# Performance work log

Hardware: AMD Instinct MI355X
Metric: run time of the kernel (lower is better)

Reference implementation:

```python
import jax, jax.numpy as jnp
import numpy as np

# Static configuration (matches init_kwargs)
L = 3264          # seq_length
K = 12            # ktc=4 -> K=12
LOCC = 4          # ktc=4 -> Locc=4
S, B, A = 8, 64, 4  # streams (user/port pairs), batch, rx antennas
DELAY_MIN, DELAY_MAX = -10, 10


def _phasor(m):
    # m: integer shifts [S, B] -> exp(1j*2*pi*m*n/L) as [S, B, L]
    n = jnp.arange(L, dtype=jnp.int32)
    ang = (2.0 * np.pi / L) * ((m[..., None] * n) % L).astype(jnp.float32)
    return jax.lax.complex(jnp.cos(ang), jnp.sin(ang))


def _linear_interp(h_avg):
    # np.interp with uniform source grid orig[i] = (LOCC-1)/2 + i*LOCC, clamped at ends.
    # h_avg: [S, B, A, R] complex, R = L // LOCC -> [S, B, A, L]
    R = L // LOCC
    new = jnp.arange(L, dtype=jnp.float32)
    t = jnp.clip((new - (LOCC - 1) / 2.0) / LOCC, 0.0, float(R - 1))
    i0 = jnp.floor(t).astype(jnp.int32)
    i1 = jnp.minimum(i0 + 1, R - 1)
    frac = (t - i0).astype(jnp.float32)
    return h_avg[..., i0] * (1.0 - frac) + h_avg[..., i1] * frac


def reference(ls_real, ls_imag, cyclic_shifts, noise_powers):
    ls = jax.lax.complex(ls_real, ls_imag)                     # [S,B,A,L]
    ideal_peak = ((K - cyclic_shifts) % K) * (L // K)          # [S]

    # Stage 1: IFFT + timing-offset search (torch.no_grad in original)
    h_time = jnp.fft.ifft(ls, axis=-1)
    power = jax.lax.stop_gradient(jnp.sum(jnp.abs(h_time) ** 2, axis=2))  # [S,B,L]
    offs = jnp.arange(DELAY_MIN, DELAY_MAX + 1, dtype=jnp.int32)          # [21]
    cand_idx = (ideal_peak[:, None] + offs[None, :]) % L                   # [S,21]
    cand_idx = jnp.broadcast_to(cand_idx[:, None, :], (S, B, offs.shape[0]))
    cand_pow = jnp.take_along_axis(power, cand_idx, axis=-1)               # [S,B,21]
    t_off = offs[jnp.argmax(cand_pow, axis=-1)]                            # [S,B]
    m = t_off + ideal_peak[:, None]                                        # [S,B]
    ph_m = _phasor(m)        # [S,B,L]
    ph_T = _phasor(t_off)    # [S,B,L]

    # Stage 2: phasor shift, OCC demux, interpolation (inside no_grad in original)
    h_shift = ls * ph_m[:, :, None, :]
    h_avg = h_shift.reshape(S, B, A, L // LOCC, LOCC).mean(-1)             # [S,B,A,L/4]
    h_interp = jax.lax.stop_gradient(_linear_interp(h_avg))                # [S,B,A,L]

    # Stage 3: global residual against stream (0,0)'s LS estimate
    total_recon = jnp.sum(h_interp * jnp.conj(ph_m)[:, :, None, :], axis=0)  # [B,A,L]
    residual = ls[0] - total_recon                                           # [B,A,L]

    # Stage 4: apply residual, MMSE (identity: mmse_module=None), timing recovery
    h_wr = h_interp + residual[None, :, :, None, :].squeeze(3) if False else h_interp + residual[None] * ph_m[:, :, None, :]
    final = h_wr * jnp.conj(ph_T)[:, :, None, :]                             # [S,B,A,L]
    return jnp.stack([final.real, final.imag]).astype(jnp.float32)          # [2,S,B,A,L]


def setup_inputs() -> dict:
    key = jax.random.key(0)
    k1, k2, k3, k4 = jax.random.split(key, 4)
    return {
        "ls_real": jax.random.normal(k1, (S, B, A, L), dtype=jnp.float32),
        "ls_imag": jax.random.normal(k2, (S, B, A, L), dtype=jnp.float32),
        "cyclic_shifts": jax.random.randint(k3, (S,), 0, K, dtype=jnp.int32),
        "noise_powers": jax.random.uniform(k4, (B,), dtype=jnp.float32),
    }
```

## Files before the change

### kernel.cpp

```cpp
#include <hip/hip_runtime.h>

namespace {

constexpr int L = 3264;
constexpr int K = 12;
constexpr int S = 8;
constexpr int B = 64;
constexpr int A = 4;
constexpr int R = 816;
constexpr int NOFF = 21;
constexpr int PEAK_STEP = L / K;
constexpr float TWO_PI = 6.28318530717958647692f;
constexpr float CINV = TWO_PI / (float)L;
constexpr int NCHUNK = (L + 255) / 256;
constexpr int HS_MAX = 66;

__device__ __forceinline__ float rfl(float x) {
    return __uint_as_float(__builtin_amdgcn_readfirstlane(__float_as_uint(x)));
}

__device__ __forceinline__ float2 cmul(float2 a, float2 b) {
    return make_float2(a.x * b.x - a.y * b.y, a.x * b.y + a.y * b.x);
}

__global__ __launch_bounds__(256)
void k_tables(const int* __restrict__ cs,
              float2* __restrict__ phT, float2* __restrict__ phI)
{
    const int g = blockIdx.x * 256 + threadIdx.x;
    if (g < NOFF * L) {
        const int t = g / L, l = g - t * L;
        int j = ((t - 10) * l) % L; if (j < 0) j += L;
        float sv, cv; __sincosf(CINV * (float)j, &sv, &cv);
        phT[g] = make_float2(cv, sv);
    } else if (g < (NOFF + S) * L) {
        const int q = g - NOFF * L;
        const int s = q / L, l = q - s * L;
        const int ideal = ((K - cs[s]) % K) * PEAK_STEP;
        const int j = (ideal * l) % L;
        float sv, cv; __sincosf(CINV * (float)j, &sv, &cv);
        phI[q] = make_float2(cv, sv);
    }
}

template <int NB>
__device__ __forceinline__ void dft_bins(
    const float* __restrict__ lscr, const float* __restrict__ lsci,
    int idx0d0, int grouplane, int lane, int w, float2 (*red)[11])
{
    const int jb = (grouplane * idx0d0) % L;
    float br, bi; __sincosf(CINV * (float)jb, &bi, &br);
    float lr, li; __sincosf(CINV * (float)grouplane, &li, &lr);
    float pwr[NB], pwi[NB], ar[NB], ai[NB];
    pwr[0] = br; pwi[0] = bi;
    #pragma unroll
    for (int d = 1; d < NB; ++d) {
        pwr[d] = pwr[d-1] * lr - pwi[d-1] * li;
        pwi[d] = pwr[d-1] * li + pwi[d-1] * lr;
    }
    #pragma unroll
    for (int d = 0; d < NB; ++d) { ar[d] = 0.f; ai[d] = 0.f; }

    const int js = (256 * idx0d0) % L;
    float s0r, s0i; __sincosf(CINV * (float)js, &s0i, &s0r);
    float c8r, c8i; __sincosf(CINV * 256.0f, &c8i, &c8r);
    float str_[NB], sti_[NB];
    {
        float cr = s0r, ci = s0i;
        #pragma unroll
        for (int d = 0; d < NB; ++d) {
            str_[d] = rfl(cr); sti_[d] = rfl(ci);
            const float nr2 = cr * c8r - ci * c8i;
            ci = cr * c8i + ci * c8r;
            cr = nr2;
        }
    }

    for (int it = 0; it < 12; ++it) {
        const int k = grouplane + (it << 8);
        const float xr = lscr[k];
        const float xi = lsci[k];
        #pragma unroll
        for (int d = 0; d < NB; ++d) {
            ar[d] += xr * pwr[d] - xi * pwi[d];
            ai[d] += xr * pwi[d] + xi * pwr[d];
            const float nr2 = pwr[d] * str_[d] - pwi[d] * sti_[d];
            pwi[d] = pwr[d] * sti_[d] + pwi[d] * str_[d];
            pwr[d] = nr2;
        }
    }
    if (grouplane < 192) {
        const float xr = lscr[grouplane + 3072];
        const float xi = lsci[grouplane + 3072];
        #pragma unroll
        for (int d = 0; d < NB; ++d) {
            ar[d] += xr * pwr[d] - xi * pwi[d];
            ai[d] += xr * pwi[d] + xi * pwr[d];
        }
    }

    #pragma unroll
    for (int d = 0; d < NB; ++d) {
        float r = ar[d], im = ai[d];
        #pragma unroll
        for (int o = 32; o > 0; o >>= 1) {
            r  += __shfl_xor(r, o);
            im += __shfl_xor(im, o);
        }
        if (lane == 0) red[w][d] = make_float2(r, im);
    }
}

__global__ __launch_bounds__(512)
void k_dft(const float* __restrict__ lsr, const float* __restrict__ lsi,
           const int* __restrict__ cs, float* __restrict__ pow_out)
{
    __shared__ float lscr[L];
    __shared__ float lsci[L];
    __shared__ float2 red[8][11];

    const int row = blockIdx.x;
    const int sb = row >> 2;
    const int a = row & 3;
    const int s = sb >> 6;
    const int tid = threadIdx.x;
    const int lane = tid & 63;
    const int w = tid >> 6;
    const int grouplane = tid & 255;
    const int grp = tid >> 8;

    {
        const float4* __restrict__ pr4 = (const float4*)(lsr + (size_t)row * L);
        const float4* __restrict__ pi4 = (const float4*)(lsi + (size_t)row * L);
        for (int idx = tid; idx < L / 4; idx += 512) {
            const float4 r4 = pr4[idx];
            const float4 i4 = pi4[idx];
            ((float4*)lscr)[idx] = r4;
            ((float4*)lsci)[idx] = i4;
        }
    }
    __syncthreads();

    const int ideal = ((K - cs[s]) % K) * PEAK_STEP;
    int idx0 = (ideal - 10) % L; if (idx0 < 0) idx0 += L;
    const int d0 = grp ? 10 : 0;
    const int idx0d0 = (idx0 + d0) % L;

    if (grp) dft_bins<11>(lscr, lsci, idx0d0, grouplane, lane, w, red);
    else     dft_bins<10>(lscr, lsci, idx0d0, grouplane, lane, w, red);
    __syncthreads();

    if (tid < NOFF) {
        const int d = tid;
        const int g = (d < 10) ? 0 : 1;
        const int dl = d - g * 10;
        float rr = 0.f, ii = 0.f;
        #pragma unroll
        for (int q = 0; q < 4; ++q) {
            rr += red[4 * g + q][dl].x;
            ii += red[4 * g + q][dl].y;
        }
        pow_out[sb * (NOFF * A) + d * A + a] = rr * rr + ii * ii;
    }
}

__global__ __launch_bounds__(64)
void k_argmax(const float* __restrict__ pow_in, const int* __restrict__ cs,
              int* __restrict__ toff_out)
{
    const int sb = blockIdx.x;
    const int lane = threadIdx.x;

    float pw = -1.f;
    if (lane < NOFF) {
        const float4 p4 = *(const float4*)(pow_in + sb * (NOFF * A) + lane * A);
        pw = p4.x + p4.y + p4.z + p4.w;
    }
    float mx = pw;
    #pragma unroll
    for (int o = 32; o > 0; o >>= 1) mx = fmaxf(mx, __shfl_xor(mx, o));
    const unsigned long long msk = __ballot(pw == mx);
    const int argd = __ffsll(msk) - 1;
    if (lane == 0) toff_out[sb] = argd - 10;
}

__global__ __launch_bounds__(256)
void k_final(const float* __restrict__ lsr, const float* __restrict__ lsi,
             const int* __restrict__ toff_arr,
             const float2* __restrict__ phT, const float2* __restrict__ phI,
             float* __restrict__ out)
{
    __shared__ float2 hs[S][HS_MAX];
    __shared__ float2 emp_s[S];
    __shared__ int tfs[S];

    const int bid = blockIdx.x;
    const int chunk = bid % NCHUNK;
    const int ba = bid / NCHUNK;
    const int b = ba >> 2;
    const int a = ba & 3;
    const int tid = threadIdx.x;

    if (tid < S) {
        const int tf = toff_arr[tid * B + b] + 10;
        tfs[tid] = tf;
        emp_s[tid] = cmul(phI[tid * L + 1], phT[tf * L + 1]);
    }
    __syncthreads();

    const int imin = max(0, chunk * 64 - 1);
    const int imax = min(R - 1, chunk * 64 + 64);
    const int cnt = imax - imin + 1;

    for (int t = tid; t < S * HS_MAX; t += 256) {
        const int s = t / HS_MAX;
        const int ii = t - s * HS_MAX;
        if (ii < cnt) {
            const int i = imin + ii;
            const int sb = s * B + b;
            const float2 emp = emp_s[s];
            float2 w2 = cmul(phI[s * L + 4 * i], phT[tfs[s] * L + 4 * i]);
            const float4 xr = *(const float4*)(lsr + ((size_t)sb * A + a) * L + 4 * i);
            const float4 xi = *(const float4*)(lsi + ((size_t)sb * A + a) * L + 4 * i);
            float wr = w2.x, wi = w2.y;
            float are, aim, nr;
            are  = xr.x * wr - xi.x * wi;  aim  = xr.x * wi + xi.x * wr;
            nr = wr * emp.x - wi * emp.y;  wi = wr * emp.y + wi * emp.x;  wr = nr;
            are += xr.y * wr - xi.y * wi;  aim += xr.y * wi + xi.y * wr;
            nr = wr * emp.x - wi * emp.y;  wi = wr * emp.y + wi * emp.x;  wr = nr;
            are += xr.z * wr - xi.z * wi;  aim += xr.z * wi + xi.z * wr;
            nr = wr * emp.x - wi * emp.y;  wi = wr * emp.y + wi * emp.x;  wr = nr;
            are += xr.w * wr - xi.w * wi;  aim += xr.w * wi + xi.w * wr;
            hs[s][ii] = make_float2(are * 0.25f, aim * 0.25f);
        }
    }
    __syncthreads();

    const int l = chunk * 256 + tid;
    if (l >= L) return;

    float t2 = ((float)l - 1.5f) * 0.25f;
    t2 = fminf(fmaxf(t2, 0.0f), (float)(R - 1));
    const int i0 = (int)t2;
    const int i1 = min(i0 + 1, R - 1);
    const float frac = t2 - (float)i0;

    float hire[S], hiim[S], pmre[S], pmim[S], ptre[S], ptim[S];
    float rre = 0.f, rim = 0.f;

    #pragma unroll
    for (int s = 0; s < S; ++s) {
        const float2 pt = phT[tfs[s] * L + l];
        const float2 wm = cmul(phI[s * L + l], pt);
        const float2 h0 = hs[s][i0 - imin];
        const float2 h1 = hs[s][i1 - imin];
        const float hr = h0.x * (1.f - frac) + h1.x * frac;
        const float hi = h0.y * (1.f - frac) + h1.y * frac;
        hire[s] = hr; hiim[s] = hi;
        pmre[s] = wm.x; pmim[s] = wm.y;
        ptre[s] = pt.x; ptim[s] = pt.y;
        rre += hr * wm.x + hi * wm.y;
        rim += hi * wm.x - hr * wm.y;
    }

    const size_t off0 = ((size_t)(b * A + a)) * L + l;
    const float resre = lsr[off0] - rre;
    const float resim = lsi[off0] - rim;

    #pragma unroll
    for (int s = 0; s < S; ++s) {
        const float wre = hire[s] + resre * pmre[s] - resim * pmim[s];
        const float wim = hiim[s] + resre * pmim[s] + resim * pmre[s];
        const float fre = wre * ptre[s] + wim * ptim[s];
        const float fim = wim * ptre[s] - wre * ptim[s];
        const size_t o = (((size_t)(s * B + b)) * A + a) * L + l;
        __builtin_nontemporal_store(fre, &out[o]);
        __builtin_nontemporal_store(fim, &out[(size_t)S * B * A * L + o]);
    }
}

}

extern "C" void kernel_launch(void* const* d_in, const int* in_sizes, int n_in,
                              void* d_out, int out_size, void* d_ws, size_t ws_size,
                              hipStream_t stream) {
    (void)in_sizes; (void)n_in; (void)out_size; (void)ws_size;
    const float* lsr = (const float*)d_in[0];
    const float* lsi = (const float*)d_in[1];
    const int*   cs  = (const int*)d_in[2];

    int* toff = (int*)d_ws;
    float2* phT  = (float2*)((char*)d_ws + 4096);
    float2* phI  = (float2*)((char*)d_ws + 4096 + 548352);
    float*  powb = (float*)((char*)d_ws + 786432);

    const int ntab = ((NOFF + S) * L + 255) / 256;
    k_tables<<<ntab, 256, 0, stream>>>(cs, phT, phI);
    k_dft   <<<S * B * A, 512, 0, stream>>>(lsr, lsi, cs, powb);
    k_argmax<<<S * B, 64, 0, stream>>>(powb, cs, toff);
    k_final <<<B * A * NCHUNK, 256, 0, stream>>>(lsr, lsi, toff, phT, phI,
                                                 (float*)d_out);
}
```

Before: 186.0 us.

## Drop shared-memory staging in DFT and final kernels, use twiddle tables

The DFT kernel no longer stages each LS row in LDS. It reads the inputs straight from global memory and builds its twiddle factors from precomputed phasor and twiddle tables (a new L-entry table is added), with per-bin steps broadcast through readlane. The final kernel drops the shared h_avg tile and its barriers, so each thread recomputes its two interpolation neighbours per stream directly from global memory. Nontemporal stores are replaced by plain stores. This removes LDS traffic and synchronisation but adds redundant global loads and arithmetic, since neighbouring threads recompute the same h_avg entries and group 0 now does 11 bins instead of 10.

```diff
diff --git a/kernel.cpp b/kernel.cpp
--- a/kernel.cpp
+++ b/kernel.cpp
@@ -13,19 +13,18 @@
 constexpr float TWO_PI = 6.28318530717958647692f;
 constexpr float CINV = TWO_PI / (float)L;
 constexpr int NCHUNK = (L + 255) / 256;
-constexpr int HS_MAX = 66;
-
-__device__ __forceinline__ float rfl(float x) {
-    return __uint_as_float(__builtin_amdgcn_readfirstlane(__float_as_uint(x)));
-}
 
 __device__ __forceinline__ float2 cmul(float2 a, float2 b) {
     return make_float2(a.x * b.x - a.y * b.y, a.x * b.y + a.y * b.x);
 }
 
+__device__ __forceinline__ float rdl(float v, int d) {
+    return __uint_as_float(__builtin_amdgcn_readlane(__float_as_uint(v), d));
+}
+
 __global__ __launch_bounds__(256)
-void k_tables(const int* __restrict__ cs,
-              float2* __restrict__ phT, float2* __restrict__ phI)
+void k_tables(const int* __restrict__ cs, float2* __restrict__ phT,
+              float2* __restrict__ phI, float2* __restrict__ tw)
 {
     const int g = blockIdx.x * 256 + threadIdx.x;
     if (g < NOFF * L) {
@@ -40,83 +39,19 @@
         const int j = (ideal * l) % L;
         float sv, cv; __sincosf(CINV * (float)j, &sv, &cv);
         phI[q] = make_float2(cv, sv);
-    }
-}
-
-template <int NB>
-__device__ __forceinline__ void dft_bins(
-    const float* __restrict__ lscr, const float* __restrict__ lsci,
-    int idx0d0, int grouplane, int lane, int w, float2 (*red)[11])
-{
-    const int jb = (grouplane * idx0d0) % L;
-    float br, bi; __sincosf(CINV * (float)jb, &bi, &br);
-    float lr, li; __sincosf(CINV * (float)grouplane, &li, &lr);
-    float pwr[NB], pwi[NB], ar[NB], ai[NB];
-    pwr[0] = br; pwi[0] = bi;
-    #pragma unroll
-    for (int d = 1; d < NB; ++d) {
-        pwr[d] = pwr[d-1] * lr - pwi[d-1] * li;
-        pwi[d] = pwr[d-1] * li + pwi[d-1] * lr;
-    }
-    #pragma unroll
-    for (int d = 0; d < NB; ++d) { ar[d] = 0.f; ai[d] = 0.f; }
-
-    const int js = (256 * idx0d0) % L;
-    float s0r, s0i; __sincosf(CINV * (float)js, &s0i, &s0r);
-    float c8r, c8i; __sincosf(CINV * 256.0f, &c8i, &c8r);
-    float str_[NB], sti_[NB];
-    {
-        float cr = s0r, ci = s0i;
-        #pragma unroll
-        for (int d = 0; d < NB; ++d) {
-            str_[d] = rfl(cr); sti_[d] = rfl(ci);
-            const float nr2 = cr * c8r - ci * c8i;
-            ci = cr * c8i + ci * c8r;
-            cr = nr2;
-        }
-    }
-
-    for (int it = 0; it < 12; ++it) {
-        const int k = grouplane + (it << 8);
-        const float xr = lscr[k];
-        const float xi = lsci[k];
-        #pragma unroll
-        for (int d = 0; d < NB; ++d) {
-            ar[d] += xr * pwr[d] - xi * pwi[d];
-            ai[d] += xr * pwi[d] + xi * pwr[d];
-            const float nr2 = pwr[d] * str_[d] - pwi[d] * sti_[d];
-            pwi[d] = pwr[d] * sti_[d] + pwi[d] * str_[d];
-            pwr[d] = nr2;
-        }
-    }
-    if (grouplane < 192) {
-        const float xr = lscr[grouplane + 3072];
-        const float xi = lsci[grouplane + 3072];
-        #pragma unroll
-        for (int d = 0; d < NB; ++d) {
-            ar[d] += xr * pwr[d] - xi * pwi[d];
-            ai[d] += xr * pwi[d] + xi * pwr[d];
-        }
-    }
-
-    #pragma unroll
-    for (int d = 0; d < NB; ++d) {
-        float r = ar[d], im = ai[d];
-        #pragma unroll
-        for (int o = 32; o > 0; o >>= 1) {
-            r  += __shfl_xor(r, o);
-            im += __shfl_xor(im, o);
-        }
-        if (lane == 0) red[w][d] = make_float2(r, im);
+    } else if (g < (NOFF + S + 1) * L) {
+        const int j = g - (NOFF + S) * L;
+        float sv, cv; __sincosf(CINV * (float)j, &sv, &cv);
+        tw[j] = make_float2(cv, sv);
     }
 }
 
 __global__ __launch_bounds__(512)
 void k_dft(const float* __restrict__ lsr, const float* __restrict__ lsi,
-           const int* __restrict__ cs, float* __restrict__ pow_out)
-{
-    __shared__ float lscr[L];
-    __shared__ float lsci[L];
+           const int* __restrict__ cs,
+           const float2* __restrict__ phT, const float2* __restrict__ phI,
+           const float2* __restrict__ tw, float* __restrict__ pow_out)
+{
     __shared__ float2 red[8][11];
 
     const int row = blockIdx.x;
@@ -126,28 +61,79 @@
     const int tid = threadIdx.x;
     const int lane = tid & 63;
     const int w = tid >> 6;
-    const int grouplane = tid & 255;
+    const int gl = tid & 255;
     const int grp = tid >> 8;
+    const int d0 = grp ? 10 : 0;
+
+    const int ideal = ((K - cs[s]) % K) * PEAK_STEP;
+    int idx0 = ideal - 10; if (idx0 < 0) idx0 += L;
+
+    const float2 w0 = cmul(phI[s * L + gl], phT[d0 * L + gl]);
+    const float2 lv = tw[gl];
 
     {
-        const float4* __restrict__ pr4 = (const float4*)(lsr + (size_t)row * L);
-        const float4* __restrict__ pi4 = (const float4*)(lsi + (size_t)row * L);
-        for (int idx = tid; idx < L / 4; idx += 512) {
-            const float4 r4 = pr4[idx];
-            const float4 i4 = pi4[idx];
-            ((float4*)lscr)[idx] = r4;
-            ((float4*)lsci)[idx] = i4;
-        }
-    }
-    __syncthreads();
-
-    const int ideal = ((K - cs[s]) % K) * PEAK_STEP;
-    int idx0 = (ideal - 10) % L; if (idx0 < 0) idx0 += L;
-    const int d0 = grp ? 10 : 0;
-    const int idx0d0 = (idx0 + d0) % L;
-
-    if (grp) dft_bins<11>(lscr, lsci, idx0d0, grouplane, lane, w, red);
-    else     dft_bins<10>(lscr, lsci, idx0d0, grouplane, lane, w, red);
+    }
+    int bidx = idx0 + d0 + (lane < 11 ? lane : 10);
+    if (bidx >= L) bidx -= L;
+    const int js = (256 * bidx) % L;
+    const float2 sv = tw[js];
+    float str_[11], sti_[11];
+    #pragma unroll
+    for (int d = 0; d < 11; ++d) {
+        str_[d] = rdl(sv.x, d);
+        sti_[d] = rdl(sv.y, d);
+    }
+
+    float pwr[11], pwi[11], ar[11], ai[11];
+    {
+        float cr = w0.x, ci = w0.y;
+        pwr[0] = cr; pwi[0] = ci;
+        #pragma unroll
+        for (int d = 1; d < 11; ++d) {
+            const float nr = cr * lv.x - ci * lv.y;
+            ci = cr * lv.y + ci * lv.x;
+            cr = nr;
+            pwr[d] = cr; pwi[d] = ci;
+        }
+    }
+    #pragma unroll
+    for (int d = 0; d < 11; ++d) { ar[d] = 0.f; ai[d] = 0.f; }
+
+    const float* __restrict__ pr  = lsr + (size_t)row * L;
+    const float* __restrict__ pi_ = lsi + (size_t)row * L;
+
+    for (int it = 0; it < 12; ++it) {
+        const float xr = pr[gl + (it << 8)];
+        const float xi = pi_[gl + (it << 8)];
+        #pragma unroll
+        for (int d = 0; d < 11; ++d) {
+            ar[d] += xr * pwr[d] - xi * pwi[d];
+            ai[d] += xr * pwi[d] + xi * pwr[d];
+            const float nr = pwr[d] * str_[d] - pwi[d] * sti_[d];
+            pwi[d] = pwr[d] * sti_[d] + pwi[d] * str_[d];
+            pwr[d] = nr;
+        }
+    }
+    if (gl < 192) {
+        const float xr = pr[gl + 3072];
+        const float xi = pi_[gl + 3072];
+        #pragma unroll
+        for (int d = 0; d < 11; ++d) {
+            ar[d] += xr * pwr[d] - xi * pwi[d];
+            ai[d] += xr * pwi[d] + xi * pwr[d];
+        }
+    }
+
+    #pragma unroll
+    for (int d = 0; d < 11; ++d) {
+        float r = ar[d], im = ai[d];
+        #pragma unroll
+        for (int o = 32; o > 0; o >>= 1) {
+            r  += __shfl_xor(r, o);
+            im += __shfl_xor(im, o);
+        }
+        if (lane == 0) red[w][d] = make_float2(r, im);
+    }
     __syncthreads();
 
     if (tid < NOFF) {
@@ -165,8 +151,7 @@
 }
 
 __global__ __launch_bounds__(64)
-void k_argmax(const float* __restrict__ pow_in, const int* __restrict__ cs,
-              int* __restrict__ toff_out)
+void k_argmax(const float* __restrict__ pow_in, int* __restrict__ toff_out)
 {
     const int sb = blockIdx.x;
     const int lane = threadIdx.x;
@@ -182,6 +167,27 @@
     const unsigned long long msk = __ballot(pw == mx);
     const int argd = __ffsll(msk) - 1;
     if (lane == 0) toff_out[sb] = argd - 10;
+}
+
+__device__ __forceinline__ float2 havg_entry(
+    const float* __restrict__ lsr, const float* __restrict__ lsi,
+    const float2* __restrict__ phT, const float2* __restrict__ phI,
+    int s, int b, int a, int tf, int i, float2 emp)
+{
+    const size_t base = ((size_t)(s * B + b) * A + a) * L + 4 * i;
+    const float4 xr = *(const float4*)(lsr + base);
+    const float4 xi = *(const float4*)(lsi + base);
+    const float2 w2 = cmul(phI[s * L + 4 * i], phT[tf * L + 4 * i]);
+    float wr = w2.x, wi = w2.y;
+    float are, aim, nr;
+    are  = xr.x * wr - xi.x * wi;  aim  = xr.x * wi + xi.x * wr;
+    nr = wr * emp.x - wi * emp.y;  wi = wr * emp.y + wi * emp.x;  wr = nr;
+    are += xr.y * wr - xi.y * wi;  aim += xr.y * wi + xi.y * wr;
+    nr = wr * emp.x - wi * emp.y;  wi = wr * emp.y + wi * emp.x;  wr = nr;
+    are += xr.z * wr - xi.z * wi;  aim += xr.z * wi + xi.z * wr;
+    nr = wr * emp.x - wi * emp.y;  wi = wr * emp.y + wi * emp.x;  wr = nr;
+    are += xr.w * wr - xi.w * wi;  aim += xr.w * wi + xi.w * wr;
+    return make_float2(are * 0.25f, aim * 0.25f);
 }
 
 __global__ __launch_bounds__(256)
@@ -190,53 +196,12 @@
              const float2* __restrict__ phT, const float2* __restrict__ phI,
              float* __restrict__ out)
 {
-    __shared__ float2 hs[S][HS_MAX];
-    __shared__ float2 emp_s[S];
-    __shared__ int tfs[S];
-
     const int bid = blockIdx.x;
     const int chunk = bid % NCHUNK;
     const int ba = bid / NCHUNK;
     const int b = ba >> 2;
     const int a = ba & 3;
-    const int tid = threadIdx.x;
-
-    if (tid < S) {
-        const int tf = toff_arr[tid * B + b] + 10;
-        tfs[tid] = tf;
-        emp_s[tid] = cmul(phI[tid * L + 1], phT[tf * L + 1]);
-    }
-    __syncthreads();
-
-    const int imin = max(0, chunk * 64 - 1);
-    const int imax = min(R - 1, chunk * 64 + 64);
-    const int cnt = imax - imin + 1;
-
-    for (int t = tid; t < S * HS_MAX; t += 256) {
-        const int s = t / HS_MAX;
-        const int ii = t - s * HS_MAX;
-        if (ii < cnt) {
-            const int i = imin + ii;
-            const int sb = s * B + b;
-            const float2 emp = emp_s[s];
-            float2 w2 = cmul(phI[s * L + 4 * i], phT[tfs[s] * L + 4 * i]);
-            const float4 xr = *(const float4*)(lsr + ((size_t)sb * A + a) * L + 4 * i);
-            const float4 xi = *(const float4*)(lsi + ((size_t)sb * A + a) * L + 4 * i);
-            float wr = w2.x, wi = w2.y;
-            float are, aim, nr;
-            are  = xr.x * wr - xi.x * wi;  aim  = xr.x * wi + xi.x * wr;
-            nr = wr * emp.x - wi * emp.y;  wi = wr * emp.y + wi * emp.x;  wr = nr;
-            are += xr.y * wr - xi.y * wi;  aim += xr.y * wi + xi.y * wr;
-            nr = wr * emp.x - wi * emp.y;  wi = wr * emp.y + wi * emp.x;  wr = nr;
-            are += xr.z * wr - xi.z * wi;  aim += xr.z * wi + xi.z * wr;
-            nr = wr * emp.x - wi * emp.y;  wi = wr * emp.y + wi * emp.x;  wr = nr;
-            are += xr.w * wr - xi.w * wi;  aim += xr.w * wi + xi.w * wr;
-            hs[s][ii] = make_float2(are * 0.25f, aim * 0.25f);
-        }
-    }
-    __syncthreads();
-
-    const int l = chunk * 256 + tid;
+    const int l = chunk * 256 + (int)threadIdx.x;
     if (l >= L) return;
 
     float t2 = ((float)l - 1.5f) * 0.25f;
@@ -250,12 +215,14 @@
 
     #pragma unroll
     for (int s = 0; s < S; ++s) {
-        const float2 pt = phT[tfs[s] * L + l];
-        const float2 wm = cmul(phI[s * L + l], pt);
-        const float2 h0 = hs[s][i0 - imin];
-        const float2 h1 = hs[s][i1 - imin];
+        const int tf = toff_arr[s * B + b] + 10;
+        const float2 emp = cmul(phI[s * L + 1], phT[tf * L + 1]);
+        const float2 h0 = havg_entry(lsr, lsi, phT, phI, s, b, a, tf, i0, emp);
+        const float2 h1 = havg_entry(lsr, lsi, phT, phI, s, b, a, tf, i1, emp);
         const float hr = h0.x * (1.f - frac) + h1.x * frac;
         const float hi = h0.y * (1.f - frac) + h1.y * frac;
+        const float2 pt = phT[tf * L + l];
+        const float2 wm = cmul(phI[s * L + l], pt);
         hire[s] = hr; hiim[s] = hi;
         pmre[s] = wm.x; pmim[s] = wm.y;
         ptre[s] = pt.x; ptim[s] = pt.y;
@@ -274,8 +241,8 @@
         const float fre = wre * ptre[s] + wim * ptim[s];
         const float fim = wim * ptre[s] - wre * ptim[s];
         const size_t o = (((size_t)(s * B + b)) * A + a) * L + l;
-        __builtin_nontemporal_store(fre, &out[o]);
-        __builtin_nontemporal_store(fim, &out[(size_t)S * B * A * L + o]);
+        out[o] = fre;
+        out[(size_t)S * B * A * L + o] = fim;
     }
 }
 
@@ -291,13 +258,14 @@
 
     int* toff = (int*)d_ws;
     float2* phT  = (float2*)((char*)d_ws + 4096);
-    float2* phI  = (float2*)((char*)d_ws + 4096 + 548352);
-    float*  powb = (float*)((char*)d_ws + 786432);
-
-    const int ntab = ((NOFF + S) * L + 255) / 256;
-    k_tables<<<ntab, 256, 0, stream>>>(cs, phT, phI);
-    k_dft   <<<S * B * A, 512, 0, stream>>>(lsr, lsi, cs, powb);
-    k_argmax<<<S * B, 64, 0, stream>>>(powb, cs, toff);
+    float2* phI  = (float2*)((char*)d_ws + 552448);
+    float2* tw   = (float2*)((char*)d_ws + 761344);
+    float*  powb = (float*)((char*)d_ws + 787456);
+
+    const int ntab = ((NOFF + S + 1) * L + 255) / 256;
+    k_tables<<<ntab, 256, 0, stream>>>(cs, phT, phI, tw);
+    k_dft   <<<S * B * A, 512, 0, stream>>>(lsr, lsi, cs, phT, phI, tw, powb);
+    k_argmax<<<S * B, 64, 0, stream>>>(powb, toff);
     k_final <<<B * A * NCHUNK, 256, 0, stream>>>(lsr, lsi, toff, phT, phI,
                                                  (float*)d_out);
 }
```

New measurement: 181.1 us. 2.6% less time.
